# Kernel tuning notes

Measured on AMD Instinct MI355X. Metric: run time of the kernel, lower is better.

## Reference

```python
import jax, jax.numpy as jnp
import numpy as np

N, E, D, B = 50000, 800000, 64, 64
NEXP, NC, EDIM, PDIM = 4, 10, 4, 100


def setup_inputs() -> dict:
    key = jax.random.key(0)
    ks = jax.random.split(key, 24)
    s = lambda f: 1.0 / np.sqrt(f)
    inp = {
        'x': jax.random.normal(ks[0], (N, D), jnp.float32),
        'edge_index': jax.random.randint(ks[1], (2, E), 0, N, jnp.int32),
        'edge_attr': jax.random.normal(ks[2], (E, EDIM), jnp.float32),
        'batch': jnp.sort(jax.random.randint(ks[3], (N,), 0, B, jnp.int32)),
        'ldxb_flag': jax.random.normal(ks[4], (B,), jnp.float32),
        # layer 1 params
        'w_edge1': jax.random.normal(ks[5], (D, EDIM)) * s(EDIM),
        'b_edge1': jnp.zeros((D,), jnp.float32),
        'w_ih1': jax.random.normal(ks[6], (3 * D, D)) * s(D),
        'w_hh1': jax.random.normal(ks[7], (3 * D, D)) * s(D),
        'b_ih1': jnp.zeros((3 * D,), jnp.float32),
        'b_hh1': jnp.zeros((3 * D,), jnp.float32),
        # layer 2 params
        'w_edge2': jax.random.normal(ks[8], (D, EDIM)) * s(EDIM),
        'b_edge2': jnp.zeros((D,), jnp.float32),
        'w_ih2': jax.random.normal(ks[9], (3 * D, D)) * s(D),
        'w_hh2': jax.random.normal(ks[10], (3 * D, D)) * s(D),
        'b_ih2': jnp.zeros((3 * D,), jnp.float32),
        'b_hh2': jnp.zeros((3 * D,), jnp.float32),
        # MoE
        'gate_w': jax.random.normal(ks[11], (NEXP, D)) * s(D),
        'gate_b': jnp.zeros((NEXP,), jnp.float32),
        'exp_w': jax.random.normal(ks[12], (NEXP, D, D)) * s(D),
        'exp_b': jnp.zeros((NEXP, D), jnp.float32),
        # heads
        'proj_w': jax.random.normal(ks[13], (PDIM, 1)),
        'proj_b': jnp.zeros((PDIM,), jnp.float32),
        'fc_w': jax.random.normal(ks[14], (NC, D + PDIM)) * s(D + PDIM),
        'fc_b': jnp.zeros((NC,), jnp.float32),
    }
    return inp


def _ggnn_layer(x, src, dst, eemb, w_ih, w_hh, b_ih, b_hh):
    # gather + scatter-add message passing (self-loops already in src/dst/eemb)
    msg = x[src] + eemb                       # [E+N, D]
    m = jnp.zeros_like(x).at[dst].add(msg)    # [N, D]
    # GRUCell(m, x): x is the hidden state
    gi = m @ w_ih.T + b_ih
    gh = x @ w_hh.T + b_hh
    i_r, i_z, i_n = jnp.split(gi, 3, axis=1)
    h_r, h_z, h_n = jnp.split(gh, 3, axis=1)
    r = jax.nn.sigmoid(i_r + h_r)
    z = jax.nn.sigmoid(i_z + h_z)
    n = jnp.tanh(i_n + r * h_n)
    return (1.0 - z) * n + z * x


def reference(x, edge_index, edge_attr, batch, ldxb_flag,
              w_edge1, b_edge1, w_ih1, w_hh1, b_ih1, b_hh1,
              w_edge2, b_edge2, w_ih2, w_hh2, b_ih2, b_hh2,
              gate_w, gate_b, exp_w, exp_b, proj_w, proj_b, fc_w, fc_b):
    n = x.shape[0]
    loop = jnp.arange(n, dtype=edge_index.dtype)
    src = jnp.concatenate([edge_index[0], loop])
    dst = jnp.concatenate([edge_index[1], loop])
    ea = jnp.concatenate([edge_attr, jnp.zeros((n, edge_attr.shape[1]), edge_attr.dtype)], axis=0)

    h = _ggnn_layer(x, src, dst, ea @ w_edge1.T + b_edge1, w_ih1, w_hh1, b_ih1, b_hh1)
    h = jax.nn.relu(h)
    h = _ggnn_layer(h, src, dst, ea @ w_edge2.T + b_edge2, w_ih2, w_hh2, b_ih2, b_hh2)
    h = jax.nn.relu(h)

    # soft MoE combine
    gw = jax.nn.softmax(h @ gate_w.T + gate_b, axis=1)            # [N, NEXP]
    eo = jax.nn.relu(jnp.einsum('nd,ehd->neh', h, exp_w) + exp_b)  # [N, NEXP, D]
    h = jnp.einsum('ne,neh->nh', gw, eo)                           # [N, D]

    # global mean pool per graph
    sums = jax.ops.segment_sum(h, batch, num_segments=B)
    cnts = jax.ops.segment_sum(jnp.ones((n,), h.dtype), batch, num_segments=B)
    graph_emb = sums / jnp.maximum(cnts, 1.0)[:, None]             # [B, D]

    flag = ldxb_flag[:, None] @ proj_w.T + proj_b                  # [B, 100]
    logits = jnp.concatenate([flag, graph_emb], axis=1) @ fc_w.T + fc_b
    return (graph_emb, graph_emb, logits)
```

## Files before the change

### kernel.cpp

```cpp
#include <hip/hip_runtime.h>
#include <stdint.h>


#define SUBCAP 8
#define OVF_MAX 32768
#define PS 16

typedef __bf16 bf16x8 __attribute__((ext_vector_type(8)));
typedef float floatx4 __attribute__((ext_vector_type(4)));
typedef unsigned short us8 __attribute__((ext_vector_type(8)));

__device__ __forceinline__ unsigned short f2bf(float f){
  union { float f; unsigned u; } c; c.f = f;
  unsigned r = c.u + 0x7FFFu + ((c.u >> 16) & 1u);
  return (unsigned short)(r >> 16);
}
__device__ __forceinline__ float bf2f(unsigned short u){
  union { unsigned u; float f; } c; c.u = ((unsigned)u) << 16; return c.f;
}
__device__ __forceinline__ float sigm(float x){ return 1.f/(1.f + __expf(-x)); }

__global__ void k_init(const float* __restrict__ s0, const float* __restrict__ s1,
                       const float* __restrict__ s2, const float* __restrict__ s3,
                       const float* __restrict__ s4, const float* __restrict__ s5,
                       unsigned short* __restrict__ dst,
                       int* __restrict__ cur, int* __restrict__ ovfcnt, int N8){
  int i = blockIdx.x*blockDim.x + threadIdx.x;
  if (i < N8) cur[i] = 0;
  if (i == 0){ ovfcnt[0] = 0; }
  if (i >= 65792) return;
  const float* s; int off;
  if      (i < 12288){ s = s0; off = i; }
  else if (i < 24576){ s = s1; off = i - 12288; }
  else if (i < 36864){ s = s2; off = i - 24576; }
  else if (i < 49152){ s = s3; off = i - 36864; }
  else if (i < 49408){ s = s4; off = i - 49152; }
  else               { s = s5; off = i - 49408; }
  dst[i] = f2bf(s[off]);
}

__global__ void k_bucket(const int* __restrict__ ei, const float* __restrict__ ea,
                         int* __restrict__ cur, int* __restrict__ bkt_src,
                         ushort4* __restrict__ bkt_ea,
                         int* __restrict__ ovfcnt, int* __restrict__ ovf,
                         int E, int N){
  int e = blockIdx.x*blockDim.x + threadIdx.x;
  if (e >= E) return;
  int sub = blockIdx.x & 7;
  int s = ei[e];
  int d = ei[E + e];
  size_t sb = (size_t)sub*N + d;
  int pos = atomicAdd(&cur[sb], 1);
  if (pos < SUBCAP){
    float4 v = *(const float4*)(ea + (size_t)e*4);
    ushort4 p; p.x = f2bf(v.x); p.y = f2bf(v.y); p.z = f2bf(v.z); p.w = f2bf(v.w);
    bkt_src[sb*SUBCAP + pos] = s;
    bkt_ea [sb*SUBCAP + pos] = p;
  } else {
    int o = atomicAdd(ovfcnt, 1);
    if (o < OVF_MAX) ovf[o] = e;
  }
}

__global__ void __launch_bounds__(256) k_gather(
    const int* __restrict__ cur, const int* __restrict__ bkt_src,
    const ushort4* __restrict__ bkt_ea,
    const float* __restrict__ xin,
    const float* __restrict__ w_edge, const float* __restrict__ b_edge,
    float* __restrict__ m, int N){
  int n = (int)(((long long)blockIdx.x*blockDim.x + threadIdx.x) >> 6);
  if (n >= N) return;
  int d = threadIdx.x & 63;
  int sub = d >> 3, k = d & 7;
  size_t sb = (size_t)sub*N + n;
  int myc = cur[sb];
  int contrib = (k == 0) ? myc : 0;
#pragma unroll
  for (int off = 1; off < 64; off <<= 1) contrib += __shfl_xor(contrib, off);
  int degAll = contrib;

  bool valid = k < min(myc, SUBCAP);
  int src = 0;
  float esx = 0.f, esy = 0.f, esz = 0.f, esw = 0.f;
  if (valid){
    src = bkt_src[sb*SUBCAP + k];
    ushort4 p = bkt_ea[sb*SUBCAP + k];
    esx = bf2f(p.x); esy = bf2f(p.y); esz = bf2f(p.z); esw = bf2f(p.w);
  }

  float4 wv = *(const float4*)(w_edge + d*4);
  float acc = xin[(size_t)n*64 + d] + (float)(degAll + 1) * b_edge[d];

  unsigned long long mm = __ballot(valid);
  while (mm){
    int l0 = (int)__builtin_ctzll(mm); mm &= mm - 1;
    int s0 = __shfl(src, l0);
    float a0 = xin[(size_t)s0*64 + d];
    float a1 = 0.f, a2 = 0.f, a3 = 0.f;
    if (mm){
      int l1 = (int)__builtin_ctzll(mm); mm &= mm - 1;
      int s1 = __shfl(src, l1);
      a1 = xin[(size_t)s1*64 + d];
      if (mm){
        int l2 = (int)__builtin_ctzll(mm); mm &= mm - 1;
        int s2 = __shfl(src, l2);
        a2 = xin[(size_t)s2*64 + d];
        if (mm){
          int l3 = (int)__builtin_ctzll(mm); mm &= mm - 1;
          int s3 = __shfl(src, l3);
          a3 = xin[(size_t)s3*64 + d];
        }
      }
    }
    acc += (a0 + a1) + (a2 + a3);
  }

#pragma unroll
  for (int off = 1; off < 64; off <<= 1){
    esx += __shfl_xor(esx, off);
    esy += __shfl_xor(esy, off);
    esz += __shfl_xor(esz, off);
    esw += __shfl_xor(esw, off);
  }
  acc += esx*wv.x + esy*wv.y + esz*wv.z + esw*wv.w;
  m[(size_t)n*64 + d] = acc;
}

__global__ void k_ovf(const int* __restrict__ ei, const float* __restrict__ ea,
                      const float* __restrict__ xin, const float* __restrict__ w_edge,
                      const int* __restrict__ ovf, const int* __restrict__ ovfcnt,
                      float* __restrict__ m, int E){
  int cnt = *ovfcnt; if (cnt > OVF_MAX) cnt = OVF_MAX;
  int nwaves = (gridDim.x * blockDim.x) >> 6;
  int wid = (int)((blockIdx.x*blockDim.x + threadIdx.x) >> 6);
  int d = threadIdx.x & 63;
  for (int k = wid; k < cnt; k += nwaves){
    int e = ovf[k];
    int s = ei[e], dst = ei[E + e];
    float4 v  = *(const float4*)(ea + (size_t)e*4);
    float4 wv = *(const float4*)(w_edge + d*4);
    float msg = xin[(size_t)s*64 + d] + v.x*wv.x + v.y*wv.y + v.z*wv.z + v.w*wv.w;
    atomicAdd(&m[(size_t)dst*64 + d], msg);
  }
}

__global__ void __launch_bounds__(256) k_gru(
    const float* __restrict__ m, const float* x,
    const unsigned short* __restrict__ wih, const unsigned short* __restrict__ whh,
    const float* __restrict__ b_ih, const float* __restrict__ b_hh,
    float* out, int tiles, int N){
  int wid = (int)(((long long)blockIdx.x*blockDim.x + threadIdx.x) >> 6);
  if (wid >= tiles) return;
  int lane = threadIdx.x & 63;
  int col = lane & 15, quad = lane >> 4;
  int na = wid*16 + col; if (na > N-1) na = N-1;

  bf16x8 am[2], ax[2];
#pragma unroll
  for (int ks = 0; ks < 2; ++ks){
    int kb = ks*32 + quad*8;
    const float4* mp = (const float4*)(m + (size_t)na*64 + kb);
    float4 lo = mp[0], hi = mp[1];
    us8 tm;
    tm[0]=f2bf(lo.x); tm[1]=f2bf(lo.y); tm[2]=f2bf(lo.z); tm[3]=f2bf(lo.w);
    tm[4]=f2bf(hi.x); tm[5]=f2bf(hi.y); tm[6]=f2bf(hi.z); tm[7]=f2bf(hi.w);
    am[ks] = __builtin_bit_cast(bf16x8, tm);
    const float4* xp = (const float4*)(x + (size_t)na*64 + kb);
    float4 xlo = xp[0], xhi = xp[1];
    us8 tx;
    tx[0]=f2bf(xlo.x); tx[1]=f2bf(xlo.y); tx[2]=f2bf(xlo.z); tx[3]=f2bf(xlo.w);
    tx[4]=f2bf(xhi.x); tx[5]=f2bf(xhi.y); tx[6]=f2bf(xhi.z); tx[7]=f2bf(xhi.w);
    ax[ks] = __builtin_bit_cast(bf16x8, tx);
  }

  floatx4 ai[12], ah[12];
#pragma unroll
  for (int nt = 0; nt < 12; ++nt){ ai[nt] = (floatx4)0.f; ah[nt] = (floatx4)0.f; }
#pragma unroll
  for (int nt = 0; nt < 12; ++nt){
    int r = nt*16 + col;
#pragma unroll
    for (int ks = 0; ks < 2; ++ks){
      int kb = ks*32 + quad*8;
      bf16x8 bi = __builtin_bit_cast(bf16x8, *(const us8*)(wih + (size_t)r*64 + kb));
      ai[nt] = __builtin_amdgcn_mfma_f32_16x16x32_bf16(am[ks], bi, ai[nt], 0,0,0);
      bf16x8 bh = __builtin_bit_cast(bf16x8, *(const us8*)(whh + (size_t)r*64 + kb));
      ah[nt] = __builtin_amdgcn_mfma_f32_16x16x32_bf16(ax[ks], bh, ah[nt], 0,0,0);
    }
  }

#pragma unroll
  for (int nt = 0; nt < 4; ++nt){
    int d = nt*16 + col;
    float bir = b_ih[d],      bhr = b_hh[d];
    float biz = b_ih[64+d],   bhz = b_hh[64+d];
    float bin = b_ih[128+d],  bhn = b_hh[128+d];
#pragma unroll
    for (int rg = 0; rg < 4; ++rg){
      int node = wid*16 + quad*4 + rg;
      if (node >= N) continue;
      float rr = sigm(ai[nt  ][rg] + bir + ah[nt  ][rg] + bhr);
      float zz = sigm(ai[nt+4][rg] + biz + ah[nt+4][rg] + bhz);
      float nn = tanhf(ai[nt+8][rg] + bin + rr*(ah[nt+8][rg] + bhn));
      float xv = x[(size_t)node*64 + d];
      float hv = (1.f - zz)*nn + zz*xv;
      out[(size_t)node*64 + d] = fmaxf(hv, 0.f);
    }
  }
}

__global__ void __launch_bounds__(256) k_moe(
    const float* __restrict__ h,
    const unsigned short* __restrict__ gate_w, const float* __restrict__ gate_b,
    const unsigned short* __restrict__ exp_w,  const float* __restrict__ exp_b,
    float* __restrict__ v_out, int tiles, int N){
  __shared__ float gsm[4][16][4];
  int gwid = (int)(((long long)blockIdx.x*blockDim.x + threadIdx.x) >> 6);
  int w = threadIdx.x >> 6;
  int lane = threadIdx.x & 63;
  int col = lane & 15, quad = lane >> 4;
  bool active = gwid < tiles;

  floatx4 accg = (floatx4)0.f;
  floatx4 acce[4][4];
#pragma unroll
  for (int e=0;e<4;++e)
#pragma unroll
    for (int nt=0;nt<4;++nt) acce[e][nt] = (floatx4)0.f;

  if (active){
    int na = gwid*16 + col; if (na > N-1) na = N-1;
    bf16x8 a[2];
#pragma unroll
    for (int ks=0; ks<2; ++ks){
      int kb = ks*32 + quad*8;
      const float4* hp = (const float4*)(h + (size_t)na*64 + kb);
      float4 lo = hp[0], hi = hp[1];
      us8 th;
      th[0]=f2bf(lo.x); th[1]=f2bf(lo.y); th[2]=f2bf(lo.z); th[3]=f2bf(lo.w);
      th[4]=f2bf(hi.x); th[5]=f2bf(hi.y); th[6]=f2bf(hi.z); th[7]=f2bf(hi.w);
      a[ks] = __builtin_bit_cast(bf16x8, th);
      us8 braw = {0,0,0,0,0,0,0,0};
      if (col < 4) braw = *(const us8*)(gate_w + col*64 + kb);
      accg = __builtin_amdgcn_mfma_f32_16x16x32_bf16(a[ks], __builtin_bit_cast(bf16x8, braw), accg, 0,0,0);
    }
#pragma unroll
    for (int e=0;e<4;++e)
#pragma unroll
      for (int nt=0;nt<4;++nt)
#pragma unroll
        for (int ks=0;ks<2;++ks){
          int kb = ks*32 + quad*8;
          bf16x8 b = __builtin_bit_cast(bf16x8,
              *(const us8*)(exp_w + ((size_t)e*64 + nt*16 + col)*64 + kb));
          acce[e][nt] = __builtin_amdgcn_mfma_f32_16x16x32_bf16(a[ks], b, acce[e][nt], 0,0,0);
        }
    if (col < 4){
      float gb = gate_b[col];
#pragma unroll
      for (int rg=0;rg<4;++rg) gsm[w][quad*4+rg][col] = accg[rg] + gb;
    }
  }
  __syncthreads();
  if (!active) return;

#pragma unroll
  for (int rg=0; rg<4; ++rg){
    int nrow = quad*4 + rg;
    int node = gwid*16 + nrow;
    if (node >= N) continue;
    float g0=gsm[w][nrow][0], g1=gsm[w][nrow][1], g2=gsm[w][nrow][2], g3=gsm[w][nrow][3];
    float mx = fmaxf(fmaxf(g0,g1), fmaxf(g2,g3));
    float e0=__expf(g0-mx), e1=__expf(g1-mx), e2=__expf(g2-mx), e3=__expf(g3-mx);
    float inv = 1.f/(e0+e1+e2+e3);
    float w0=e0*inv, w1=e1*inv, w2=e2*inv, w3=e3*inv;
#pragma unroll
    for (int nt=0;nt<4;++nt){
      int o = nt*16 + col;
      float v = w0*fmaxf(acce[0][nt][rg] + exp_b[      o], 0.f)
              + w1*fmaxf(acce[1][nt][rg] + exp_b[ 64 + o], 0.f)
              + w2*fmaxf(acce[2][nt][rg] + exp_b[128 + o], 0.f)
              + w3*fmaxf(acce[3][nt][rg] + exp_b[192 + o], 0.f);
      v_out[(size_t)node*64 + o] = v;
    }
  }
}

__device__ __forceinline__ int lower_bound_i(const int* __restrict__ a, int n, int key){
  int lo = 0, hi = n;
  while (lo < hi){ int mid = (lo + hi) >> 1; if (a[mid] < key) lo = mid + 1; else hi = mid; }
  return lo;
}

__global__ void __launch_bounds__(256) k_pool(
    const float* __restrict__ v, const int* __restrict__ batch, int N,
    float* __restrict__ partial){
  __shared__ float red[4][64];
  int g = blockIdx.x / PS, s = blockIdx.x % PS;
  int t = threadIdx.x, d = t & 63, r = t >> 6;
  int start = lower_bound_i(batch, N, g);
  int end   = lower_bound_i(batch, N, g + 1);
  int len = end - start;
  int per = (len + PS - 1) / PS;
  int s0 = start + s*per;
  int s1 = s0 + per; if (s1 > end) s1 = end;
  float acc = 0.f;
  for (int i = s0 + r; i < s1; i += 4)
    acc += v[(size_t)i*64 + d];
  red[r][d] = acc;
  __syncthreads();
  if (r == 0)
    partial[(size_t)blockIdx.x*64 + d] = red[0][d] + red[1][d] + red[2][d] + red[3][d];
}

__global__ void __launch_bounds__(64) k_head(
    const float* __restrict__ partial, const int* __restrict__ batch, int N, int B,
    const float* __restrict__ ldxb,
    const float* __restrict__ proj_w, const float* __restrict__ proj_b,
    const float* __restrict__ fc_w, const float* __restrict__ fc_b,
    float* __restrict__ out){
  __shared__ float ges[64];
  int b = blockIdx.x, d = threadIdx.x;
  int start = lower_bound_i(batch, N, b);
  int end   = lower_bound_i(batch, N, b + 1);
  float sum = 0.f;
#pragma unroll
  for (int s = 0; s < PS; ++s)
    sum += partial[((size_t)b*PS + s)*64 + d];
  float ge = sum / fmaxf((float)(end - start), 1.f);
  ges[d] = ge;
  out[(size_t)b*64 + d]                = ge;
  out[(size_t)B*64 + (size_t)b*64 + d] = ge;
  __syncthreads();
  if (d < 10){
    float acc = fc_b[d];
    float fl = ldxb[b];
    const float* fr = fc_w + d*164;
    for (int p = 0; p < 100; ++p) acc += (fl*proj_w[p] + proj_b[p]) * fr[p];
    for (int dd = 0; dd < 64; ++dd) acc += ges[dd]*fr[100 + dd];
    out[(size_t)B*128 + (size_t)b*10 + d] = acc;
  }
}

extern "C" void kernel_launch(void* const* d_in, const int* in_sizes, int n_in,
                              void* d_out, int out_size, void* d_ws, size_t ws_size,
                              hipStream_t stream){
  const float* x      = (const float*)d_in[0];
  const int*   ei     = (const int*)d_in[1];
  const float* ea     = (const float*)d_in[2];
  const int*   batch  = (const int*)d_in[3];
  const float* ldxb   = (const float*)d_in[4];
  const float* w_edge1= (const float*)d_in[5];
  const float* b_edge1= (const float*)d_in[6];
  const float* w_ih1  = (const float*)d_in[7];
  const float* w_hh1  = (const float*)d_in[8];
  const float* b_ih1  = (const float*)d_in[9];
  const float* b_hh1  = (const float*)d_in[10];
  const float* w_edge2= (const float*)d_in[11];
  const float* b_edge2= (const float*)d_in[12];
  const float* w_ih2  = (const float*)d_in[13];
  const float* w_hh2  = (const float*)d_in[14];
  const float* b_ih2  = (const float*)d_in[15];
  const float* b_hh2  = (const float*)d_in[16];
  const float* gate_w = (const float*)d_in[17];
  const float* gate_b = (const float*)d_in[18];
  const float* exp_w  = (const float*)d_in[19];
  const float* exp_b  = (const float*)d_in[20];
  const float* proj_w = (const float*)d_in[21];
  const float* proj_b = (const float*)d_in[22];
  const float* fc_w   = (const float*)d_in[23];
  const float* fc_b   = (const float*)d_in[24];
  float* out = (float*)d_out;

  int N = in_sizes[0] / 64;
  int E = in_sizes[1] / 2;
  int B = in_sizes[4];
  int tiles = (N + 15) / 16;
  int nTot = N * 64;

  float*   m       = (float*)d_ws;
  float*   h       = m + (size_t)nTot;
  int*     bkt_src = (int*)(h + (size_t)nTot);
  ushort4* bkt_ea  = (ushort4*)(bkt_src + (size_t)nTot);
  int*     cur     = (int*)(bkt_ea + (size_t)nTot);
  int*     ovfcnt  = cur + (size_t)N*8;
  int*     ovf     = ovfcnt + 4;
  unsigned short* wbf = (unsigned short*)(ovf + OVF_MAX);
  float*   partial = (float*)(wbf + 65792);
  unsigned short* wih1bf = wbf;
  unsigned short* whh1bf = wbf + 12288;
  unsigned short* wih2bf = wbf + 24576;
  unsigned short* whh2bf = wbf + 36864;
  unsigned short* gatebf = wbf + 49152;
  unsigned short* expbf  = wbf + 49408;

  dim3 blk(256);
  int edgeBlocks = (E + 255)/256;
  int nodeWaveBlocks = (N + 3)/4;
  int waveBlocks = (tiles + 3)/4;
  int N8 = N*8;
  int initBlocks = ((N8 > 65792 ? N8 : 65792) + 255)/256;

  k_init<<<initBlocks, blk, 0, stream>>>(w_ih1, w_hh1, w_ih2, w_hh2, gate_w, exp_w,
                                         wbf, cur, ovfcnt, N8);
  k_bucket<<<edgeBlocks, blk, 0, stream>>>(ei, ea, cur, bkt_src, bkt_ea, ovfcnt, ovf, E, N);
  k_gather<<<nodeWaveBlocks, blk, 0, stream>>>(cur, bkt_src, bkt_ea, x, w_edge1, b_edge1, m, N);
  k_ovf<<<8, blk, 0, stream>>>(ei, ea, x, w_edge1, ovf, ovfcnt, m, E);
  k_gru<<<waveBlocks, blk, 0, stream>>>(m, x, wih1bf, whh1bf, b_ih1, b_hh1, h, tiles, N);
  k_gather<<<nodeWaveBlocks, blk, 0, stream>>>(cur, bkt_src, bkt_ea, h, w_edge2, b_edge2, m, N);
  k_ovf<<<8, blk, 0, stream>>>(ei, ea, h, w_edge2, ovf, ovfcnt, m, E);
  k_gru<<<waveBlocks, blk, 0, stream>>>(m, h, wih2bf, whh2bf, b_ih2, b_hh2, h, tiles, N);
  k_moe<<<waveBlocks, blk, 0, stream>>>(h, gatebf, gate_b, expbf, exp_b, m, tiles, N);
  k_pool<<<B*PS, blk, 0, stream>>>(m, batch, N, partial);
  k_head<<<B, 64, 0, stream>>>(partial, batch, N, B, ldxb, proj_w, proj_b, fc_w, fc_b, out);
}
```

Baseline: 365.7 us.

## Split GRU and MoE tiles across four waves per block

k_gru and k_moe now give each 16-node tile to a whole 256-thread block instead of a single wave. In k_gru each wave computes one 16-column slice of the r/z/n gates, with a barrier so that in-place output writes cannot overwrite inputs other waves still need. In k_moe each wave computes one expert, and the four weighted expert outputs are summed through shared memory before a single store. The aim is fewer live accumulator registers per wave, hence better occupancy and more latency hiding, at the cost of each wave reloading the tile's activation rows and the added barriers and shared-memory traffic.

```diff
diff --git a/kernel.cpp b/kernel.cpp
--- a/kernel.cpp
+++ b/kernel.cpp
@@ -149,11 +149,12 @@
     const unsigned short* __restrict__ wih, const unsigned short* __restrict__ whh,
     const float* __restrict__ b_ih, const float* __restrict__ b_hh,
     float* out, int tiles, int N){
-  int wid = (int)(((long long)blockIdx.x*blockDim.x + threadIdx.x) >> 6);
-  if (wid >= tiles) return;
+  int tile = blockIdx.x;
+  if (tile >= tiles) return;
+  int j    = threadIdx.x >> 6;
   int lane = threadIdx.x & 63;
   int col = lane & 15, quad = lane >> 4;
-  int na = wid*16 + col; if (na > N-1) na = N-1;
+  int na = tile*16 + col; if (na > N-1) na = N-1;
 
   bf16x8 am[2], ax[2];
 #pragma unroll
@@ -172,40 +173,38 @@
     tx[4]=f2bf(xhi.x); tx[5]=f2bf(xhi.y); tx[6]=f2bf(xhi.z); tx[7]=f2bf(xhi.w);
     ax[ks] = __builtin_bit_cast(bf16x8, tx);
   }
-
-  floatx4 ai[12], ah[12];
-#pragma unroll
-  for (int nt = 0; nt < 12; ++nt){ ai[nt] = (floatx4)0.f; ah[nt] = (floatx4)0.f; }
-#pragma unroll
-  for (int nt = 0; nt < 12; ++nt){
-    int r = nt*16 + col;
+  __syncthreads();
+
+  floatx4 ai[3], ah[3];
+#pragma unroll
+  for (int g = 0; g < 3; ++g){ ai[g] = (floatx4)0.f; ah[g] = (floatx4)0.f; }
+#pragma unroll
+  for (int g = 0; g < 3; ++g){
+    int r = (g*4 + j)*16 + col;
 #pragma unroll
     for (int ks = 0; ks < 2; ++ks){
       int kb = ks*32 + quad*8;
       bf16x8 bi = __builtin_bit_cast(bf16x8, *(const us8*)(wih + (size_t)r*64 + kb));
-      ai[nt] = __builtin_amdgcn_mfma_f32_16x16x32_bf16(am[ks], bi, ai[nt], 0,0,0);
+      ai[g] = __builtin_amdgcn_mfma_f32_16x16x32_bf16(am[ks], bi, ai[g], 0,0,0);
       bf16x8 bh = __builtin_bit_cast(bf16x8, *(const us8*)(whh + (size_t)r*64 + kb));
-      ah[nt] = __builtin_amdgcn_mfma_f32_16x16x32_bf16(ax[ks], bh, ah[nt], 0,0,0);
-    }
-  }
-
-#pragma unroll
-  for (int nt = 0; nt < 4; ++nt){
-    int d = nt*16 + col;
-    float bir = b_ih[d],      bhr = b_hh[d];
-    float biz = b_ih[64+d],   bhz = b_hh[64+d];
-    float bin = b_ih[128+d],  bhn = b_hh[128+d];
-#pragma unroll
-    for (int rg = 0; rg < 4; ++rg){
-      int node = wid*16 + quad*4 + rg;
-      if (node >= N) continue;
-      float rr = sigm(ai[nt  ][rg] + bir + ah[nt  ][rg] + bhr);
-      float zz = sigm(ai[nt+4][rg] + biz + ah[nt+4][rg] + bhz);
-      float nn = tanhf(ai[nt+8][rg] + bin + rr*(ah[nt+8][rg] + bhn));
-      float xv = x[(size_t)node*64 + d];
-      float hv = (1.f - zz)*nn + zz*xv;
-      out[(size_t)node*64 + d] = fmaxf(hv, 0.f);
-    }
+      ah[g] = __builtin_amdgcn_mfma_f32_16x16x32_bf16(ax[ks], bh, ah[g], 0,0,0);
+    }
+  }
+
+  int d = j*16 + col;
+  float bir = b_ih[d],      bhr = b_hh[d];
+  float biz = b_ih[64+d],   bhz = b_hh[64+d];
+  float bin = b_ih[128+d],  bhn = b_hh[128+d];
+#pragma unroll
+  for (int rg = 0; rg < 4; ++rg){
+    int node = tile*16 + quad*4 + rg;
+    if (node >= N) continue;
+    float rr = sigm(ai[0][rg] + bir + ah[0][rg] + bhr);
+    float zz = sigm(ai[1][rg] + biz + ah[1][rg] + bhz);
+    float nn = tanhf(ai[2][rg] + bin + rr*(ah[2][rg] + bhn));
+    float xv = x[(size_t)node*64 + d];
+    float hv = (1.f - zz)*nn + zz*xv;
+    out[(size_t)node*64 + d] = fmaxf(hv, 0.f);
   }
 }
 
@@ -214,75 +213,78 @@
     const unsigned short* __restrict__ gate_w, const float* __restrict__ gate_b,
     const unsigned short* __restrict__ exp_w,  const float* __restrict__ exp_b,
     float* __restrict__ v_out, int tiles, int N){
-  __shared__ float gsm[4][16][4];
-  int gwid = (int)(((long long)blockIdx.x*blockDim.x + threadIdx.x) >> 6);
-  int w = threadIdx.x >> 6;
+  __shared__ float gsm[16][4];
+  __shared__ float vsm[4][16][65];
+  int tile = blockIdx.x;
+  if (tile >= tiles) return;
+  int e    = threadIdx.x >> 6;
   int lane = threadIdx.x & 63;
   int col = lane & 15, quad = lane >> 4;
-  bool active = gwid < tiles;
-
-  floatx4 accg = (floatx4)0.f;
-  floatx4 acce[4][4];
-#pragma unroll
-  for (int e=0;e<4;++e)
-#pragma unroll
-    for (int nt=0;nt<4;++nt) acce[e][nt] = (floatx4)0.f;
-
-  if (active){
-    int na = gwid*16 + col; if (na > N-1) na = N-1;
-    bf16x8 a[2];
+  int na = tile*16 + col; if (na > N-1) na = N-1;
+
+  bf16x8 a[2];
+#pragma unroll
+  for (int ks=0; ks<2; ++ks){
+    int kb = ks*32 + quad*8;
+    const float4* hp = (const float4*)(h + (size_t)na*64 + kb);
+    float4 lo = hp[0], hi = hp[1];
+    us8 th;
+    th[0]=f2bf(lo.x); th[1]=f2bf(lo.y); th[2]=f2bf(lo.z); th[3]=f2bf(lo.w);
+    th[4]=f2bf(hi.x); th[5]=f2bf(hi.y); th[6]=f2bf(hi.z); th[7]=f2bf(hi.w);
+    a[ks] = __builtin_bit_cast(bf16x8, th);
+  }
+
+  if (e == 0){
+    floatx4 accg = (floatx4)0.f;
 #pragma unroll
     for (int ks=0; ks<2; ++ks){
       int kb = ks*32 + quad*8;
-      const float4* hp = (const float4*)(h + (size_t)na*64 + kb);
-      float4 lo = hp[0], hi = hp[1];
-      us8 th;
-      th[0]=f2bf(lo.x); th[1]=f2bf(lo.y); th[2]=f2bf(lo.z); th[3]=f2bf(lo.w);
-      th[4]=f2bf(hi.x); th[5]=f2bf(hi.y); th[6]=f2bf(hi.z); th[7]=f2bf(hi.w);
-      a[ks] = __builtin_bit_cast(bf16x8, th);
       us8 braw = {0,0,0,0,0,0,0,0};
       if (col < 4) braw = *(const us8*)(gate_w + col*64 + kb);
       accg = __builtin_amdgcn_mfma_f32_16x16x32_bf16(a[ks], __builtin_bit_cast(bf16x8, braw), accg, 0,0,0);
     }
-#pragma unroll
-    for (int e=0;e<4;++e)
-#pragma unroll
-      for (int nt=0;nt<4;++nt)
-#pragma unroll
-        for (int ks=0;ks<2;++ks){
-          int kb = ks*32 + quad*8;
-          bf16x8 b = __builtin_bit_cast(bf16x8,
-              *(const us8*)(exp_w + ((size_t)e*64 + nt*16 + col)*64 + kb));
-          acce[e][nt] = __builtin_amdgcn_mfma_f32_16x16x32_bf16(a[ks], b, acce[e][nt], 0,0,0);
-        }
     if (col < 4){
       float gb = gate_b[col];
 #pragma unroll
-      for (int rg=0;rg<4;++rg) gsm[w][quad*4+rg][col] = accg[rg] + gb;
-    }
-  }
+      for (int rg=0;rg<4;++rg) gsm[quad*4+rg][col] = accg[rg] + gb;
+    }
+  }
+
+  floatx4 acc[4];
+#pragma unroll
+  for (int nt=0;nt<4;++nt) acc[nt] = (floatx4)0.f;
+#pragma unroll
+  for (int nt=0;nt<4;++nt)
+#pragma unroll
+    for (int ks=0;ks<2;++ks){
+      int kb = ks*32 + quad*8;
+      bf16x8 b = __builtin_bit_cast(bf16x8,
+          *(const us8*)(exp_w + ((size_t)e*64 + nt*16 + col)*64 + kb));
+      acc[nt] = __builtin_amdgcn_mfma_f32_16x16x32_bf16(a[ks], b, acc[nt], 0,0,0);
+    }
   __syncthreads();
-  if (!active) return;
 
 #pragma unroll
   for (int rg=0; rg<4; ++rg){
     int nrow = quad*4 + rg;
-    int node = gwid*16 + nrow;
-    if (node >= N) continue;
-    float g0=gsm[w][nrow][0], g1=gsm[w][nrow][1], g2=gsm[w][nrow][2], g3=gsm[w][nrow][3];
+    float g0=gsm[nrow][0], g1=gsm[nrow][1], g2=gsm[nrow][2], g3=gsm[nrow][3];
     float mx = fmaxf(fmaxf(g0,g1), fmaxf(g2,g3));
     float e0=__expf(g0-mx), e1=__expf(g1-mx), e2=__expf(g2-mx), e3=__expf(g3-mx);
-    float inv = 1.f/(e0+e1+e2+e3);
-    float w0=e0*inv, w1=e1*inv, w2=e2*inv, w3=e3*inv;
+    float we = ((e==0)?e0:(e==1)?e1:(e==2)?e2:e3) / (e0+e1+e2+e3);
 #pragma unroll
     for (int nt=0;nt<4;++nt){
       int o = nt*16 + col;
-      float v = w0*fmaxf(acce[0][nt][rg] + exp_b[      o], 0.f)
-              + w1*fmaxf(acce[1][nt][rg] + exp_b[ 64 + o], 0.f)
-              + w2*fmaxf(acce[2][nt][rg] + exp_b[128 + o], 0.f)
-              + w3*fmaxf(acce[3][nt][rg] + exp_b[192 + o], 0.f);
-      v_out[(size_t)node*64 + o] = v;
-    }
+      vsm[e][nrow][o] = we * fmaxf(acc[nt][rg] + exp_b[e*64 + o], 0.f);
+    }
+  }
+  __syncthreads();
+
+  for (int idx = threadIdx.x; idx < 1024; idx += 256){
+    int nrow = idx >> 6, o = idx & 63;
+    int node = tile*16 + nrow;
+    if (node < N)
+      v_out[(size_t)node*64 + o] = vsm[0][nrow][o] + vsm[1][nrow][o]
+                                 + vsm[2][nrow][o] + vsm[3][nrow][o];
   }
 }
 
@@ -397,7 +399,6 @@
   dim3 blk(256);
   int edgeBlocks = (E + 255)/256;
   int nodeWaveBlocks = (N + 3)/4;
-  int waveBlocks = (tiles + 3)/4;
   int N8 = N*8;
   int initBlocks = ((N8 > 65792 ? N8 : 65792) + 255)/256;
 
@@ -406,11 +407,11 @@
   k_bucket<<<edgeBlocks, blk, 0, stream>>>(ei, ea, cur, bkt_src, bkt_ea, ovfcnt, ovf, E, N);
   k_gather<<<nodeWaveBlocks, blk, 0, stream>>>(cur, bkt_src, bkt_ea, x, w_edge1, b_edge1, m, N);
   k_ovf<<<8, blk, 0, stream>>>(ei, ea, x, w_edge1, ovf, ovfcnt, m, E);
-  k_gru<<<waveBlocks, blk, 0, stream>>>(m, x, wih1bf, whh1bf, b_ih1, b_hh1, h, tiles, N);
+  k_gru<<<tiles, blk, 0, stream>>>(m, x, wih1bf, whh1bf, b_ih1, b_hh1, h, tiles, N);
   k_gather<<<nodeWaveBlocks, blk, 0, stream>>>(cur, bkt_src, bkt_ea, h, w_edge2, b_edge2, m, N);
   k_ovf<<<8, blk, 0, stream>>>(ei, ea, h, w_edge2, ovf, ovfcnt, m, E);
-  k_gru<<<waveBlocks, blk, 0, stream>>>(m, h, wih2bf, whh2bf, b_ih2, b_hh2, h, tiles, N);
-  k_moe<<<waveBlocks, blk, 0, stream>>>(h, gatebf, gate_b, expbf, exp_b, m, tiles, N);
+  k_gru<<<tiles, blk, 0, stream>>>(m, h, wih2bf, whh2bf, b_ih2, b_hh2, h, tiles, N);
+  k_moe<<<tiles, blk, 0, stream>>>(h, gatebf, gate_b, expbf, exp_b, m, tiles, N);
   k_pool<<<B*PS, blk, 0, stream>>>(m, batch, N, partial);
   k_head<<<B, 64, 0, stream>>>(partial, batch, N, B, ldxb, proj_w, proj_b, fc_w, fc_b, out);
 }
```

Result: no change. 362.6 us (-0.8%).
